# Kernel tuning notes

Hardware: AMD Instinct MI355X
Metric: run time of the kernel (lower is better)

Reference implementation:

```python
import jax, jax.numpy as jnp
import numpy as np

B, S, D_IN, H, D_K = 4, 2048, 512, 8, 64
EPS = 1e-5

def _layer_norm(x, gamma, beta):
    mu = jnp.mean(x, axis=-1, keepdims=True)
    var = jnp.var(x, axis=-1, keepdims=True)
    return (x - mu) * jax.lax.rsqrt(var + EPS) * gamma + beta

def setup_inputs() -> dict:
    key = jax.random.key(0)
    ks = jax.random.split(key, 8)
    d_model = H * D_K
    scale = 1.0 / np.sqrt(D_IN)
    inp = {
        "q": jax.random.normal(ks[0], (B, S, D_IN), jnp.float32),
        "k": jax.random.normal(ks[1], (B, S, D_IN), jnp.float32),
        "v": jax.random.normal(ks[2], (B, S, D_IN), jnp.float32),
        "mask": jnp.ones((B, 1, S, S), jnp.float32),
        "Wq": jax.random.normal(ks[3], (D_IN, d_model), jnp.float32) * scale,
        "bq": jnp.zeros((d_model,), jnp.float32),
        "Wk": jax.random.normal(ks[4], (D_IN, d_model), jnp.float32) * scale,
        "bk": jnp.zeros((d_model,), jnp.float32),
        "Wv": jax.random.normal(ks[5], (D_IN, d_model), jnp.float32) * scale,
        "bv": jnp.zeros((d_model,), jnp.float32),
        "Wo": jax.random.normal(ks[6], (d_model, D_IN), jnp.float32) * (1.0 / np.sqrt(d_model)),
        "bo": jnp.zeros((D_IN,), jnp.float32),
        "gamma": jnp.ones((D_IN,), jnp.float32),
        "beta": jnp.zeros((D_IN,), jnp.float32),
    }
    return inp

def reference(q, k, v, mask, Wq, bq, Wk, bk, Wv, bv, Wo, bo, gamma, beta):
    b, sq, _ = q.shape
    # QKV projections, split heads: [B,S,H*Dk] -> [B,H,S,Dk]
    qh = (q @ Wq + bq).reshape(b, sq, H, D_K).transpose(0, 2, 1, 3)
    kh = (k @ Wk + bk).reshape(b, -1, H, D_K).transpose(0, 2, 1, 3)
    vh = (v @ Wv + bv).reshape(b, -1, H, D_K).transpose(0, 2, 1, 3)
    # scores with multiplicative mask + threshold (non-standard, per source)
    scores = jnp.einsum('bhqd,bhkd->bhqk', qh, kh) / np.sqrt(D_K)
    scores = scores * mask  # mask broadcasts over heads (repeat in torch)
    scores = jnp.where(scores > 0, scores, jnp.float32(-10000.0))
    attn = jax.nn.softmax(scores, axis=-1)
    out = jnp.einsum('bhqk,bhkd->bhqd', attn, vh)
    out = out.transpose(0, 2, 1, 3).reshape(b, sq, H * D_K)
    out = out @ Wo + bo
    return _layer_norm(q + out, gamma, beta)
```

## Files before the change

kernel.cpp:

```cpp
#include <hip/hip_runtime.h>
#include <stdint.h>

typedef __attribute__((ext_vector_type(8))) short s16x8;
typedef __attribute__((ext_vector_type(4))) float f32x4;

__device__ __forceinline__ unsigned short f2bf(float f){
  union { float f; unsigned u; } v; v.f = f;
  return (unsigned short)((v.u + 0x7FFFu + ((v.u>>16)&1u))>>16);
}
__device__ __forceinline__ float bf2f(unsigned short u){
  union { unsigned u; float f; } c; c.u = ((unsigned)u)<<16; return c.f;
}
#if __has_builtin(__builtin_amdgcn_cvt_pk_bf16_f32)
__device__ __forceinline__ unsigned pkbf(float a, float b){
  typedef __attribute__((ext_vector_type(2))) __bf16 bf16x2;
  union { bf16x2 v; unsigned u; } c;
  c.v = __builtin_amdgcn_cvt_pk_bf16_f32(a, b);
  return c.u;
}
#else
__device__ __forceinline__ unsigned pkbf(float a, float b){
  return (unsigned)f2bf(a) | ((unsigned)f2bf(b)<<16);
}
#endif

__device__ __forceinline__ void g2l16(const void* g, void* l){
  auto* lp = reinterpret_cast<__attribute__((address_space(3))) unsigned int*>(
      reinterpret_cast<uintptr_t>(l));
  auto* gp = reinterpret_cast<const __attribute__((address_space(1))) unsigned int*>(
      reinterpret_cast<uintptr_t>(g));
  __builtin_amdgcn_global_load_lds(gp, lp, 16, 0, 0);
}

__global__ __launch_bounds__(256) void prep_all(
    const float* __restrict__ mask, const float* __restrict__ q,
    const float* __restrict__ k,    const float* __restrict__ v,
    const float* __restrict__ W0, const float* __restrict__ W1,
    const float* __restrict__ W2, const float* __restrict__ W3,
    unsigned short* __restrict__ mo, unsigned short* __restrict__ qo,
    unsigned short* __restrict__ ko, unsigned short* __restrict__ vo,
    unsigned short* __restrict__ T0, unsigned short* __restrict__ T1,
    unsigned short* __restrict__ T2, unsigned short* __restrict__ T3)
{
  const int z = blockIdx.z;
  const int t = threadIdx.x;
  if (z == 4){
    if (blockIdx.x >= 256) return;
    __shared__ float Ts[64][65];
    const int wid = blockIdx.x >> 6, within = blockIdx.x & 63;
    const float* W = (wid==0)?W0:(wid==1)?W1:(wid==2)?W2:W3;
    unsigned short* Wt = (wid==0)?T0:(wid==1)?T1:(wid==2)?T2:T3;
    const int k0 = (within>>3)*64, n0 = (within&7)*64;
    {
      const int r = t>>4, c = (t&15)*4;
#pragma unroll
      for (int rr=0; rr<4; ++rr){
        const float4 w4 = *(const float4*)&W[(size_t)(k0 + r + rr*16)*512 + n0 + c];
        Ts[r+rr*16][c]   = w4.x; Ts[r+rr*16][c+1] = w4.y;
        Ts[r+rr*16][c+2] = w4.z; Ts[r+rr*16][c+3] = w4.w;
      }
    }
    __syncthreads();
    const int n = t>>2, kc = (t&3)*16;
    unsigned o[8];
#pragma unroll
    for (int i=0;i<16;i+=2) o[i>>1] = pkbf(Ts[kc+i][n], Ts[kc+i+1][n]);
    *(uint4*)&Wt[(size_t)(n0+n)*512 + k0 + kc]     = *(uint4*)&o[0];
    *(uint4*)&Wt[(size_t)(n0+n)*512 + k0 + kc + 8] = *(uint4*)&o[4];
    return;
  }
  const float* src = (z==0)?mask:(z==1)?q:(z==2)?k:v;
  unsigned short* dst = (z==0)?mo:(z==1)?qo:(z==2)?ko:vo;
  const int nblk = (z==0) ? 8192 : 2048;
  if (blockIdx.x >= nblk) return;
  const size_t i8 = ((size_t)blockIdx.x*256 + t)*8;
  const float4 a = *(const float4*)&src[i8];
  const float4 b = *(const float4*)&src[i8+4];
  uint4 o;
  o.x = pkbf(a.x,a.y); o.y = pkbf(a.z,a.w);
  o.z = pkbf(b.x,b.y); o.w = pkbf(b.z,b.w);
  *(uint4*)&dst[i8] = o;
}

template<int EPI>
__global__ __launch_bounds__(256) void gemm_m97(
    const unsigned short* __restrict__ A0, const unsigned short* __restrict__ A1,
    const unsigned short* __restrict__ A2,
    const unsigned short* __restrict__ W0, const unsigned short* __restrict__ W1,
    const unsigned short* __restrict__ W2,
    const float* __restrict__ b0, const float* __restrict__ b1, const float* __restrict__ b2,
    unsigned short* __restrict__ Oq, unsigned short* __restrict__ Ok,
    unsigned short* __restrict__ Ov, unsigned short* __restrict__ Oflat)
{
  __shared__ unsigned short SM[2*128*64];
  unsigned short* As = SM;
  unsigned short* Bs = SM + 128*64;
  const int t = threadIdx.x;
  const int lane = t & 63;
  const int w = t >> 6;
  const int l16 = lane & 15;
  const int quad = lane >> 4;
  const int wm = w & 1, wn = w >> 1;
  const int bm = blockIdx.x, bn = blockIdx.y;
  const int z = (EPI==0) ? (int)blockIdx.z : 0;
  const unsigned short* A  = (z==0)?A0:(z==1)?A1:A2;
  const unsigned short* Wt = (z==0)?W0:(z==1)?W1:W2;
  const float* bias        = (z==0)?b0:(z==1)?b1:b2;

  const int Lr = lane >> 3;
  const int gc = (lane & 7) ^ Lr;

  f32x4 acc[4][4];
#pragma unroll
  for(int i=0;i<4;i++)
#pragma unroll
    for(int j=0;j<4;j++) acc[i][j] = (f32x4){0.f,0.f,0.f,0.f};

  for (int kt=0; kt<8; ++kt){
    const int k0 = kt*64;
#pragma unroll
    for (int j=0;j<4;++j){
      const int rb = w*32 + j*8;
      g2l16(&A [(size_t)(bm*128 + rb + Lr)*512 + k0 + gc*8], &As[rb*64]);
      g2l16(&Wt[(size_t)(bn*128 + rb + Lr)*512 + k0 + gc*8], &Bs[rb*64]);
    }
    __syncthreads();
#pragma unroll
    for (int kk=0;kk<2;++kk){
      s16x8 af[4], bfr[4];
#pragma unroll
      for (int mt=0;mt<4;++mt){
        const int row = wm*64 + mt*16 + l16;
        af[mt] = *(const s16x8*)&As[row*64 + (((kk*4+quad) ^ (row&7))*8)];
      }
#pragma unroll
      for (int nt=0;nt<4;++nt){
        const int row = wn*64 + nt*16 + l16;
        bfr[nt] = *(const s16x8*)&Bs[row*64 + (((kk*4+quad) ^ (row&7))*8)];
      }
#pragma unroll
      for (int mt=0;mt<4;++mt)
#pragma unroll
        for (int nt=0;nt<4;++nt)
          acc[mt][nt] = __builtin_amdgcn_mfma_f32_16x16x32_bf16(af[mt], bfr[nt], acc[mt][nt], 0,0,0);
    }
    __syncthreads();
  }

  if (EPI==0 && z==2){
#pragma unroll
    for (int mt=0;mt<4;++mt){
      const int gm = bm*128 + wm*64 + mt*16 + quad*4;
      const int b_ = gm>>11, s = gm & 2047;
#pragma unroll
      for (int nt=0;nt<4;++nt){
        const int gn = bn*128 + wn*64 + nt*16 + l16;
        const float bv = bias[gn];
        const int hh = gn>>6, dk = gn&63;
        uint2 uu;
        uu.x = pkbf(acc[mt][nt][0]+bv, acc[mt][nt][1]+bv);
        uu.y = pkbf(acc[mt][nt][2]+bv, acc[mt][nt][3]+bv);
        *(uint2*)&Ov[(((size_t)b_*8 + hh)*64 + dk)*2048 + s] = uu;
      }
    }
    return;
  }

  const float scl = (EPI==0 && z==0) ? 0.125f : 1.0f;
#pragma unroll
  for (int mt=0;mt<4;++mt){
    const int rl = wm*64 + mt*16 + quad*4;
#pragma unroll
    for (int nt=0;nt<4;++nt){
      const int cl = wn*64 + nt*16 + l16;
      const float bv = bias[bn*128 + cl];
#pragma unroll
      for (int r=0;r<4;++r)
        SM[(rl+r)*128 + cl] = f2bf((acc[mt][nt][r] + bv)*scl);
    }
  }
  __syncthreads();
#pragma unroll
  for (int i=0;i<8;++i){
    const int u = t*8 + i;
    const int row = u >> 4, seg = u & 15;
    const uint4 val = *(const uint4*)&SM[row*128 + seg*8];
    if (EPI==1){
      *(uint4*)&Oflat[(size_t)(bm*128+row)*512 + bn*128 + seg*8] = val;
    } else {
      const int col = bn*128 + seg*8;
      const int hh = col>>6, dk = col&63;
      const int gm2 = bm*128 + row;
      const int b_ = gm2>>11, s = gm2&2047;
      unsigned short* Out = (z==0)?Oq:Ok;
      *(uint4*)&Out[(((size_t)b_*8 + hh)*2048 + s)*64 + dk] = val;
    }
  }
}

__global__ __launch_bounds__(512,4) void attn_kernel(
    const unsigned short* __restrict__ Qp, const unsigned short* __restrict__ Kp,
    const unsigned short* __restrict__ Vt, const unsigned short* __restrict__ maskb,
    unsigned short* __restrict__ Ap)
{
  __shared__ unsigned short Ks[2][8*512];
  __shared__ unsigned short Vs[2][8*528];
  const int t = threadIdx.x;
  const int lane = t & 63;
  const int w = t >> 6;
  const int l16 = lane & 15;
  const int quad = lane >> 4;
  const int g = blockIdx.x;
  const int h = blockIdx.y;
  const int qt = g & 15, b = g >> 4;
  const int q0 = qt*128 + w*16;
  const unsigned short* Qb = Qp + ((size_t)b*8 + h)*2048*64;
  const unsigned short* Kb = Kp + ((size_t)b*8 + h)*2048*64;
  const unsigned short* Vb = Vt + ((size_t)b*8 + h)*64*2048;
  const unsigned short* mb = maskb + (size_t)b*2048*2048 + (size_t)(q0 + l16)*2048 + quad*4;

  s16x8 qf[2];
#pragma unroll
  for (int kk=0;kk<2;++kk)
    qf[kk] = *(const s16x8*)&Qb[(size_t)(q0 + l16)*64 + kk*32 + quad*8];

  const int koff = (((w>>1)*16 + l16)*64) + (((w&1)*4 + quad)*8);
  const int voff = ((w*8 + (lane>>3))*2048) + (((lane&7) ^ (lane>>3))*8);

  g2l16(Kb + koff, &Ks[0][w*512]);
  g2l16(Vb + voff, &Vs[0][w*528]);
  uint2 mcur[4], mnext[4];
#pragma unroll
  for (int nt=0;nt<4;++nt) mcur[nt] = *(const uint2*)&mb[nt*16];

  f32x4 o_acc[4];
#pragma unroll
  for(int nt=0;nt<4;++nt) o_acc[nt]=(f32x4){0.f,0.f,0.f,0.f};
  float l_run = 0.f;

  const int b3 = l16>>3, a7 = l16&7;
  union U8 { unsigned u[4]; s16x8 v; };

  for (int kt=0; kt<32; ++kt){
    const int cur = kt&1;
    __syncthreads();

    if (kt<31){
      const int kb2 = (kt+1)*64;
      g2l16(Kb + (size_t)kb2*64 + koff, &Ks[cur^1][w*512]);
      g2l16(Vb + kb2 + voff,            &Vs[cur^1][w*528]);
#pragma unroll
      for (int nt=0;nt<4;++nt) mnext[nt] = *(const uint2*)&mb[kb2 + nt*16];
    }

    f32x4 sc[4];
#pragma unroll
    for(int nt=0;nt<4;++nt) sc[nt]=(f32x4){0.f,0.f,0.f,0.f};
#pragma unroll
    for (int nt=0;nt<4;++nt)
#pragma unroll
      for (int kk=0;kk<2;++kk){
        const s16x8 kf = *(const s16x8*)&Ks[cur][(nt*2+kk)*512 + lane*8];
        sc[nt] = __builtin_amdgcn_mfma_f32_16x16x32_bf16(kf, qf[kk], sc[nt],0,0,0);
      }

    unsigned pk[8];
    float rs = 0.f;
#pragma unroll
    for (int nt=0;nt<4;++nt){
      const float m0 = bf2f((unsigned short)(mcur[nt].x & 0xffffu));
      const float m1 = bf2f((unsigned short)(mcur[nt].x >> 16));
      const float m2 = bf2f((unsigned short)(mcur[nt].y & 0xffffu));
      const float m3 = bf2f((unsigned short)(mcur[nt].y >> 16));
      float x0 = sc[nt][0]*m0, x1 = sc[nt][1]*m1, x2 = sc[nt][2]*m2, x3 = sc[nt][3]*m3;
      x0 = (x0>0.f)?x0:-10000.f; x1 = (x1>0.f)?x1:-10000.f;
      x2 = (x2>0.f)?x2:-10000.f; x3 = (x3>0.f)?x3:-10000.f;
      const float e0 = __expf(x0), e1 = __expf(x1), e2 = __expf(x2), e3 = __expf(x3);
      rs += (e0+e1)+(e2+e3);
      pk[nt*2]   = pkbf(e0, e1);
      pk[nt*2+1] = pkbf(e2, e3);
    }
    rs += __shfl_xor(rs, 16);
    rs += __shfl_xor(rs, 32);
    l_run += rs;
    U8 pu[2];
#pragma unroll
    for (int kk=0;kk<2;++kk)
#pragma unroll
      for (int c=0;c<4;++c){
        const int srcLane = (((quad&1)*2 + (c>>1))<<4) | l16;
        const int vA = __shfl((int)pk[kk*4 + (c&1)],     srcLane);
        const int vB = __shfl((int)pk[kk*4 + 2 + (c&1)], srcLane);
        pu[kk].u[c] = (quad < 2) ? (unsigned)vA : (unsigned)vB;
      }
#pragma unroll
    for (int ot=0;ot<4;++ot){
#pragma unroll
      for (int kk=0;kk<2;++kk){
        const s16x8 vf = *(const s16x8*)&Vs[cur][(ot*2+b3)*528 + a7*64 + (((kk*4+quad)^a7)*8)];
        o_acc[ot] = __builtin_amdgcn_mfma_f32_16x16x32_bf16(vf, pu[kk].v, o_acc[ot],0,0,0);
      }
    }
#pragma unroll
    for (int nt=0;nt<4;++nt) mcur[nt] = mnext[nt];
  }

  {
    const float inv = 1.0f / l_run;
    const int gq = q0 + l16;
#pragma unroll
    for (int ot=0;ot<4;++ot){
      uint2 uu;
      uu.x = pkbf(o_acc[ot][0]*inv, o_acc[ot][1]*inv);
      uu.y = pkbf(o_acc[ot][2]*inv, o_acc[ot][3]*inv);
      *(uint2*)&Ap[((size_t)b*2048 + gq)*512 + h*64 + ot*16 + quad*4] = uu;
    }
  }
}

__global__ __launch_bounds__(256) void ln_kernel(
    const float* __restrict__ q, const unsigned short* __restrict__ O2,
    const float* __restrict__ gamma, const float* __restrict__ beta,
    float* __restrict__ out)
{
  const int r = blockIdx.x;
  const int t = threadIdx.x;
  const float* xq = q + (size_t)r * 512;
  const unsigned short* xo = O2 + (size_t)r * 512;
  const float x0 = xq[t]       + bf2f(xo[t]);
  const float x1 = xq[t + 256] + bf2f(xo[t + 256]);
  float s  = x0 + x1;
  float ss = x0*x0 + x1*x1;
#pragma unroll
  for (int off = 1; off < 64; off <<= 1) {
    s  += __shfl_xor(s, off);
    ss += __shfl_xor(ss, off);
  }
  __shared__ float ssum[4], ssq[4];
  const int w = t >> 6;
  if ((t & 63) == 0) { ssum[w] = s; ssq[w] = ss; }
  __syncthreads();
  const float S4 = ssum[0] + ssum[1] + ssum[2] + ssum[3];
  const float Q4 = ssq[0] + ssq[1] + ssq[2] + ssq[3];
  const float mu   = S4 * (1.0f / 512.0f);
  const float var  = Q4 * (1.0f / 512.0f) - mu * mu;
  const float rstd = rsqrtf(var + 1e-5f);
  out[(size_t)r*512 + t]       = (x0 - mu)*rstd*gamma[t] + beta[t];
  out[(size_t)r*512 + t + 256] = (x1 - mu)*rstd*gamma[t+256] + beta[t+256];
}

extern "C" void kernel_launch(void* const* d_in, const int* in_sizes, int n_in,
                              void* d_out, int out_size, void* d_ws, size_t ws_size,
                              hipStream_t stream)
{
  (void)in_sizes; (void)n_in; (void)out_size; (void)ws_size;
  const float* q    = (const float*)d_in[0];
  const float* k    = (const float*)d_in[1];
  const float* v    = (const float*)d_in[2];
  const float* mask = (const float*)d_in[3];
  const float* Wq   = (const float*)d_in[4];
  const float* bq   = (const float*)d_in[5];
  const float* Wk   = (const float*)d_in[6];
  const float* bk   = (const float*)d_in[7];
  const float* Wv   = (const float*)d_in[8];
  const float* bv   = (const float*)d_in[9];
  const float* Wo   = (const float*)d_in[10];
  const float* bo   = (const float*)d_in[11];
  const float* gamma = (const float*)d_in[12];
  const float* beta  = (const float*)d_in[13];
  float* out = (float*)d_out;

  const size_t NT = (size_t)8192*512;
  unsigned short* WtQ  = (unsigned short*)d_ws;
  unsigned short* WtK  = WtQ + 512*512;
  unsigned short* WtV  = WtK + 512*512;
  unsigned short* WtO  = WtV + 512*512;
  unsigned short* Mb   = WtO + 512*512;
  unsigned short* qb   = Mb + (size_t)4*2048*2048;
  unsigned short* kb   = qb + NT;
  unsigned short* vb   = kb + NT;
  unsigned short* Qp   = vb + NT;
  unsigned short* Kp   = Qp + NT;
  unsigned short* Vtg  = Kp + NT;
  unsigned short* Ap   = Vtg + NT;
  unsigned short* O2b  = Ap + NT;

  prep_all<<<dim3(8192,1,5), 256, 0, stream>>>(mask, q, k, v, Wq, Wk, Wv, Wo,
                                               Mb, qb, kb, vb, WtQ, WtK, WtV, WtO);
  gemm_m97<0><<<dim3(64,4,3), 256, 0, stream>>>(qb, kb, vb, WtQ, WtK, WtV,
                                                bq, bk, bv, Qp, Kp, Vtg, nullptr);
  attn_kernel<<<dim3(64,8), 512, 0, stream>>>(Qp, Kp, Vtg, Mb, Ap);
  gemm_m97<1><<<dim3(64,4,1), 256, 0, stream>>>(Ap, nullptr, nullptr, WtO, nullptr, nullptr,
                                                bo, nullptr, nullptr,
                                                nullptr, nullptr, nullptr, O2b);
  ln_kernel<<<dim3(8192), 256, 0, stream>>>(q, O2b, gamma, beta, out);
}
```

Baseline: 305.1 us.

## Double-buffer GEMM loads, widen attention warps to two query tiles, use exp2

The projection GEMM now prefetches the next K-slice into a second LDS buffer while computing on the current one, which removes one barrier per iteration. The attention kernel now runs 256 threads, each wave covering 32 query rows instead of 16, so every K and V fragment read from LDS feeds two MFMAs. Its mask is read in 16-byte chunks. The softmax now uses exp2 with log2(e) folded into the bf16 mask during prep, and masked entries are set to zero directly instead of computing exp(-10000). In exchange, each wave uses more registers and there are fewer waves per block, and the folded scale adds bf16 rounding error to the mask.

```diff
diff --git a/kernel.cpp b/kernel.cpp
--- a/kernel.cpp
+++ b/kernel.cpp
@@ -22,6 +22,11 @@
 __device__ __forceinline__ unsigned pkbf(float a, float b){
   return (unsigned)f2bf(a) | ((unsigned)f2bf(b)<<16);
 }
+#endif
+#if __has_builtin(__builtin_amdgcn_exp2f)
+__device__ __forceinline__ float fexp2(float x){ return __builtin_amdgcn_exp2f(x); }
+#else
+__device__ __forceinline__ float fexp2(float x){ return exp2f(x); }
 #endif
 
 __device__ __forceinline__ void g2l16(const void* g, void* l){
@@ -73,17 +78,18 @@
   unsigned short* dst = (z==0)?mo:(z==1)?qo:(z==2)?ko:vo;
   const int nblk = (z==0) ? 8192 : 2048;
   if (blockIdx.x >= nblk) return;
+  const float scl = (z==0) ? 1.4426950408889634f : 1.0f;
   const size_t i8 = ((size_t)blockIdx.x*256 + t)*8;
   const float4 a = *(const float4*)&src[i8];
   const float4 b = *(const float4*)&src[i8+4];
   uint4 o;
-  o.x = pkbf(a.x,a.y); o.y = pkbf(a.z,a.w);
-  o.z = pkbf(b.x,b.y); o.w = pkbf(b.z,b.w);
+  o.x = pkbf(a.x*scl,a.y*scl); o.y = pkbf(a.z*scl,a.w*scl);
+  o.z = pkbf(b.x*scl,b.y*scl); o.w = pkbf(b.z*scl,b.w*scl);
   *(uint4*)&dst[i8] = o;
 }
 
 template<int EPI>
-__global__ __launch_bounds__(256) void gemm_m97(
+__global__ __launch_bounds__(256) void gemm_db(
     const unsigned short* __restrict__ A0, const unsigned short* __restrict__ A1,
     const unsigned short* __restrict__ A2,
     const unsigned short* __restrict__ W0, const unsigned short* __restrict__ W1,
@@ -92,9 +98,7 @@
     unsigned short* __restrict__ Oq, unsigned short* __restrict__ Ok,
     unsigned short* __restrict__ Ov, unsigned short* __restrict__ Oflat)
 {
-  __shared__ unsigned short SM[2*128*64];
-  unsigned short* As = SM;
-  unsigned short* Bs = SM + 128*64;
+  __shared__ unsigned short SM[4*128*64];
   const int t = threadIdx.x;
   const int lane = t & 63;
   const int w = t >> 6;
@@ -116,15 +120,28 @@
 #pragma unroll
     for(int j=0;j<4;j++) acc[i][j] = (f32x4){0.f,0.f,0.f,0.f};
 
+#pragma unroll
+  for (int j=0;j<4;++j){
+    const int rb = w*32 + j*8;
+    g2l16(&A [(size_t)(bm*128 + rb + Lr)*512 + gc*8], &SM[0*8192 + rb*64]);
+    g2l16(&Wt[(size_t)(bn*128 + rb + Lr)*512 + gc*8], &SM[1*8192 + rb*64]);
+  }
+
   for (int kt=0; kt<8; ++kt){
-    const int k0 = kt*64;
-#pragma unroll
-    for (int j=0;j<4;++j){
-      const int rb = w*32 + j*8;
-      g2l16(&A [(size_t)(bm*128 + rb + Lr)*512 + k0 + gc*8], &As[rb*64]);
-      g2l16(&Wt[(size_t)(bn*128 + rb + Lr)*512 + k0 + gc*8], &Bs[rb*64]);
-    }
+    const int cur = kt&1;
     __syncthreads();
+    if (kt<7){
+      const int k0 = (kt+1)*64;
+      const int nb = (cur^1)*2;
+#pragma unroll
+      for (int j=0;j<4;++j){
+        const int rb = w*32 + j*8;
+        g2l16(&A [(size_t)(bm*128 + rb + Lr)*512 + k0 + gc*8], &SM[(size_t)nb*8192 + rb*64]);
+        g2l16(&Wt[(size_t)(bn*128 + rb + Lr)*512 + k0 + gc*8], &SM[(size_t)(nb+1)*8192 + rb*64]);
+      }
+    }
+    const unsigned short* As = &SM[(size_t)cur*2*8192];
+    const unsigned short* Bs = As + 8192;
 #pragma unroll
     for (int kk=0;kk<2;++kk){
       s16x8 af[4], bfr[4];
@@ -144,7 +161,6 @@
         for (int nt=0;nt<4;++nt)
           acc[mt][nt] = __builtin_amdgcn_mfma_f32_16x16x32_bf16(af[mt], bfr[nt], acc[mt][nt], 0,0,0);
     }
-    __syncthreads();
   }
 
   if (EPI==0 && z==2){
@@ -198,7 +214,7 @@
   }
 }
 
-__global__ __launch_bounds__(512,4) void attn_kernel(
+__global__ __launch_bounds__(256,2) void attn_kernel(
     const unsigned short* __restrict__ Qp, const unsigned short* __restrict__ Kp,
     const unsigned short* __restrict__ Vt, const unsigned short* __restrict__ maskb,
     unsigned short* __restrict__ Ap)
@@ -213,30 +229,49 @@
   const int g = blockIdx.x;
   const int h = blockIdx.y;
   const int qt = g & 15, b = g >> 4;
-  const int q0 = qt*128 + w*16;
+  const int q0w = qt*128 + w*32;
   const unsigned short* Qb = Qp + ((size_t)b*8 + h)*2048*64;
   const unsigned short* Kb = Kp + ((size_t)b*8 + h)*2048*64;
   const unsigned short* Vb = Vt + ((size_t)b*8 + h)*64*2048;
-  const unsigned short* mb = maskb + (size_t)b*2048*2048 + (size_t)(q0 + l16)*2048 + quad*4;
-
-  s16x8 qf[2];
-#pragma unroll
-  for (int kk=0;kk<2;++kk)
-    qf[kk] = *(const s16x8*)&Qb[(size_t)(q0 + l16)*64 + kk*32 + quad*8];
-
-  const int koff = (((w>>1)*16 + l16)*64) + (((w&1)*4 + quad)*8);
-  const int voff = ((w*8 + (lane>>3))*2048) + (((lane&7) ^ (lane>>3))*8);
-
-  g2l16(Kb + koff, &Ks[0][w*512]);
-  g2l16(Vb + voff, &Vs[0][w*528]);
-  uint2 mcur[4], mnext[4];
-#pragma unroll
-  for (int nt=0;nt<4;++nt) mcur[nt] = *(const uint2*)&mb[nt*16];
-
-  f32x4 o_acc[4];
-#pragma unroll
-  for(int nt=0;nt<4;++nt) o_acc[nt]=(f32x4){0.f,0.f,0.f,0.f};
-  float l_run = 0.f;
+  const unsigned short* mb = maskb + (size_t)b*2048*2048;
+
+  s16x8 qf[2][2];
+#pragma unroll
+  for (int tc=0;tc<2;++tc)
+#pragma unroll
+    for (int kap=0;kap<2;++kap)
+      qf[tc][kap] = *(const s16x8*)&Qb[(size_t)(q0w + tc*16 + l16)*64 + kap*32 + quad*8];
+
+  int koffs[2], voffs[2];
+#pragma unroll
+  for (int j=0;j<2;++j){
+    const int f = 2*w + j;
+    const int kkb = f>>2, pair = (f>>1)&1, kap = f&1;
+    const int row = kkb*32 + (l16>>2)*8 + pair*4 + (l16&3);
+    koffs[j] = row*64 + kap*32 + quad*8;
+    const int gg = 2*w + j;
+    voffs[j] = ((gg*8 + (lane>>3))*2048) + (((lane&7) ^ (lane>>3))*8);
+  }
+#pragma unroll
+  for (int j=0;j<2;++j){
+    g2l16(Kb + koffs[j], &Ks[0][(2*w+j)*512]);
+    g2l16(Vb + voffs[j], &Vs[0][(2*w+j)*528]);
+  }
+  const unsigned short* mrow[2] = {
+    mb + (size_t)(q0w +      l16)*2048 + quad*8,
+    mb + (size_t)(q0w + 16 + l16)*2048 + quad*8 };
+  uint4 mcur[2][2], mnext[2][2];
+#pragma unroll
+  for (int tc=0;tc<2;++tc)
+#pragma unroll
+    for (int kkb=0;kkb<2;++kkb) mcur[tc][kkb] = *(const uint4*)&mrow[tc][kkb*32];
+
+  f32x4 o_acc[2][4];
+#pragma unroll
+  for(int tc=0;tc<2;++tc)
+#pragma unroll
+    for(int ot=0;ot<4;++ot) o_acc[tc][ot]=(f32x4){0.f,0.f,0.f,0.f};
+  float l_run[2] = {0.f, 0.f};
 
   const int b3 = l16>>3, a7 = l16&7;
   union U8 { unsigned u[4]; s16x8 v; };
@@ -247,72 +282,93 @@
 
     if (kt<31){
       const int kb2 = (kt+1)*64;
-      g2l16(Kb + (size_t)kb2*64 + koff, &Ks[cur^1][w*512]);
-      g2l16(Vb + kb2 + voff,            &Vs[cur^1][w*528]);
-#pragma unroll
-      for (int nt=0;nt<4;++nt) mnext[nt] = *(const uint2*)&mb[kb2 + nt*16];
-    }
-
-    f32x4 sc[4];
-#pragma unroll
-    for(int nt=0;nt<4;++nt) sc[nt]=(f32x4){0.f,0.f,0.f,0.f};
-#pragma unroll
-    for (int nt=0;nt<4;++nt)
-#pragma unroll
-      for (int kk=0;kk<2;++kk){
-        const s16x8 kf = *(const s16x8*)&Ks[cur][(nt*2+kk)*512 + lane*8];
-        sc[nt] = __builtin_amdgcn_mfma_f32_16x16x32_bf16(kf, qf[kk], sc[nt],0,0,0);
-      }
-
-    unsigned pk[8];
-    float rs = 0.f;
-#pragma unroll
-    for (int nt=0;nt<4;++nt){
-      const float m0 = bf2f((unsigned short)(mcur[nt].x & 0xffffu));
-      const float m1 = bf2f((unsigned short)(mcur[nt].x >> 16));
-      const float m2 = bf2f((unsigned short)(mcur[nt].y & 0xffffu));
-      const float m3 = bf2f((unsigned short)(mcur[nt].y >> 16));
-      float x0 = sc[nt][0]*m0, x1 = sc[nt][1]*m1, x2 = sc[nt][2]*m2, x3 = sc[nt][3]*m3;
-      x0 = (x0>0.f)?x0:-10000.f; x1 = (x1>0.f)?x1:-10000.f;
-      x2 = (x2>0.f)?x2:-10000.f; x3 = (x3>0.f)?x3:-10000.f;
-      const float e0 = __expf(x0), e1 = __expf(x1), e2 = __expf(x2), e3 = __expf(x3);
-      rs += (e0+e1)+(e2+e3);
-      pk[nt*2]   = pkbf(e0, e1);
-      pk[nt*2+1] = pkbf(e2, e3);
-    }
-    rs += __shfl_xor(rs, 16);
-    rs += __shfl_xor(rs, 32);
-    l_run += rs;
-    U8 pu[2];
-#pragma unroll
-    for (int kk=0;kk<2;++kk)
-#pragma unroll
-      for (int c=0;c<4;++c){
-        const int srcLane = (((quad&1)*2 + (c>>1))<<4) | l16;
-        const int vA = __shfl((int)pk[kk*4 + (c&1)],     srcLane);
-        const int vB = __shfl((int)pk[kk*4 + 2 + (c&1)], srcLane);
-        pu[kk].u[c] = (quad < 2) ? (unsigned)vA : (unsigned)vB;
-      }
-#pragma unroll
-    for (int ot=0;ot<4;++ot){
-#pragma unroll
-      for (int kk=0;kk<2;++kk){
-        const s16x8 vf = *(const s16x8*)&Vs[cur][(ot*2+b3)*528 + a7*64 + (((kk*4+quad)^a7)*8)];
-        o_acc[ot] = __builtin_amdgcn_mfma_f32_16x16x32_bf16(vf, pu[kk].v, o_acc[ot],0,0,0);
-      }
-    }
-#pragma unroll
-    for (int nt=0;nt<4;++nt) mcur[nt] = mnext[nt];
-  }
-
-  {
-    const float inv = 1.0f / l_run;
-    const int gq = q0 + l16;
+#pragma unroll
+      for (int j=0;j<2;++j){
+        g2l16(Kb + (size_t)kb2*64 + koffs[j], &Ks[cur^1][(2*w+j)*512]);
+        g2l16(Vb + kb2 + voffs[j],            &Vs[cur^1][(2*w+j)*528]);
+      }
+#pragma unroll
+      for (int tc=0;tc<2;++tc)
+#pragma unroll
+        for (int kkb=0;kkb<2;++kkb) mnext[tc][kkb] = *(const uint4*)&mrow[tc][kb2 + kkb*32];
+    }
+
+    f32x4 sc[2][2][2];
+#pragma unroll
+    for(int tc=0;tc<2;++tc)
+#pragma unroll
+      for(int kkb=0;kkb<2;++kkb)
+#pragma unroll
+        for(int pp=0;pp<2;++pp) sc[tc][kkb][pp]=(f32x4){0.f,0.f,0.f,0.f};
+#pragma unroll
+    for (int kkb=0;kkb<2;++kkb)
+#pragma unroll
+      for (int pp=0;pp<2;++pp)
+#pragma unroll
+        for (int kap=0;kap<2;++kap){
+          const s16x8 kf = *(const s16x8*)&Ks[cur][(kkb*4+pp*2+kap)*512 + lane*8];
+#pragma unroll
+          for (int tc=0;tc<2;++tc)
+            sc[tc][kkb][pp] = __builtin_amdgcn_mfma_f32_16x16x32_bf16(kf, qf[tc][kap], sc[tc][kkb][pp],0,0,0);
+        }
+
+    U8 pu[2][2];
+#pragma unroll
+    for (int tc=0;tc<2;++tc){
+      float rs = 0.f;
+#pragma unroll
+      for (int kkb=0;kkb<2;++kkb){
+        const uint4 m = mcur[tc][kkb];
+        const float m0 = bf2f((unsigned short)(m.x & 0xffffu));
+        const float m1 = bf2f((unsigned short)(m.x >> 16));
+        const float m2 = bf2f((unsigned short)(m.y & 0xffffu));
+        const float m3 = bf2f((unsigned short)(m.y >> 16));
+        const float m4 = bf2f((unsigned short)(m.z & 0xffffu));
+        const float m5 = bf2f((unsigned short)(m.z >> 16));
+        const float m6 = bf2f((unsigned short)(m.w & 0xffffu));
+        const float m7 = bf2f((unsigned short)(m.w >> 16));
+        const f32x4 sa = sc[tc][kkb][0], sb = sc[tc][kkb][1];
+        const float xa0 = sa[0]*m0, xa1 = sa[1]*m1, xa2 = sa[2]*m2, xa3 = sa[3]*m3;
+        const float xb0 = sb[0]*m4, xb1 = sb[1]*m5, xb2 = sb[2]*m6, xb3 = sb[3]*m7;
+        const float pa0 = (xa0>0.f)?fexp2(xa0):0.f, pa1 = (xa1>0.f)?fexp2(xa1):0.f;
+        const float pa2 = (xa2>0.f)?fexp2(xa2):0.f, pa3 = (xa3>0.f)?fexp2(xa3):0.f;
+        const float pb0 = (xb0>0.f)?fexp2(xb0):0.f, pb1 = (xb1>0.f)?fexp2(xb1):0.f;
+        const float pb2 = (xb2>0.f)?fexp2(xb2):0.f, pb3 = (xb3>0.f)?fexp2(xb3):0.f;
+        rs += ((pa0+pa1)+(pa2+pa3)) + ((pb0+pb1)+(pb2+pb3));
+        pu[tc][kkb].u[0] = pkbf(pa0, pa1);
+        pu[tc][kkb].u[1] = pkbf(pa2, pa3);
+        pu[tc][kkb].u[2] = pkbf(pb0, pb1);
+        pu[tc][kkb].u[3] = pkbf(pb2, pb3);
+      }
+      rs += __shfl_xor(rs, 16);
+      rs += __shfl_xor(rs, 32);
+      l_run[tc] += rs;
+    }
+
+#pragma unroll
+    for (int ot=0;ot<4;++ot)
+#pragma unroll
+      for (int kkb=0;kkb<2;++kkb){
+        const s16x8 vf = *(const s16x8*)&Vs[cur][(ot*2+b3)*528 + a7*64 + (((kkb*4+quad)^a7)*8)];
+#pragma unroll
+        for (int tc=0;tc<2;++tc)
+          o_acc[tc][ot] = __builtin_amdgcn_mfma_f32_16x16x32_bf16(vf, pu[tc][kkb].v, o_acc[tc][ot],0,0,0);
+      }
+#pragma unroll
+    for (int tc=0;tc<2;++tc)
+#pragma unroll
+      for (int kkb=0;kkb<2;++kkb) mcur[tc][kkb] = mnext[tc][kkb];
+  }
+
+#pragma unroll
+  for (int tc=0;tc<2;++tc){
+    const float inv = 1.0f / l_run[tc];
+    const int gq = q0w + tc*16 + l16;
 #pragma unroll
     for (int ot=0;ot<4;++ot){
       uint2 uu;
-      uu.x = pkbf(o_acc[ot][0]*inv, o_acc[ot][1]*inv);
-      uu.y = pkbf(o_acc[ot][2]*inv, o_acc[ot][3]*inv);
+      uu.x = pkbf(o_acc[tc][ot][0]*inv, o_acc[tc][ot][1]*inv);
+      uu.y = pkbf(o_acc[tc][ot][2]*inv, o_acc[tc][ot][3]*inv);
       *(uint2*)&Ap[((size_t)b*2048 + gq)*512 + h*64 + ot*16 + quad*4] = uu;
     }
   }
@@ -387,11 +443,11 @@
 
   prep_all<<<dim3(8192,1,5), 256, 0, stream>>>(mask, q, k, v, Wq, Wk, Wv, Wo,
                                                Mb, qb, kb, vb, WtQ, WtK, WtV, WtO);
-  gemm_m97<0><<<dim3(64,4,3), 256, 0, stream>>>(qb, kb, vb, WtQ, WtK, WtV,
-                                                bq, bk, bv, Qp, Kp, Vtg, nullptr);
-  attn_kernel<<<dim3(64,8), 512, 0, stream>>>(Qp, Kp, Vtg, Mb, Ap);
-  gemm_m97<1><<<dim3(64,4,1), 256, 0, stream>>>(Ap, nullptr, nullptr, WtO, nullptr, nullptr,
-                                                bo, nullptr, nullptr,
-                                                nullptr, nullptr, nullptr, O2b);
+  gemm_db<0><<<dim3(64,4,3), 256, 0, stream>>>(qb, kb, vb, WtQ, WtK, WtV,
+                                               bq, bk, bv, Qp, Kp, Vtg, nullptr);
+  attn_kernel<<<dim3(64,8), 256, 0, stream>>>(Qp, Kp, Vtg, Mb, Ap);
+  gemm_db<1><<<dim3(64,4,1), 256, 0, stream>>>(Ap, nullptr, nullptr, WtO, nullptr, nullptr,
+                                               bo, nullptr, nullptr,
+                                               nullptr, nullptr, nullptr, O2b);
   ln_kernel<<<dim3(8192), 256, 0, stream>>>(q, O2b, gamma, beta, out);
 }
```

New measurement: 283.5 us. -7.1%, faster.
